# Performance work log

Measured on AMD Instinct MI355X. Metric: run time of the kernel, lower is better.

Reference implementation:

```python
import jax, jax.numpy as jnp
import numpy as np

T, H, I, E, TOPK = 4096, 2048, 4096, 8, 2


def setup_inputs() -> dict:
    key = jax.random.key(0)
    k0, k1, k2, k3, k4, k5 = jax.random.split(key, 6)
    return {
        "hidden_states": jax.random.normal(k0, (T, H), dtype=jnp.float32),
        "expert_affinities": jax.random.uniform(k1, (T, E), dtype=jnp.float32),
        "expert_index": jax.random.randint(k2, (T, TOPK), 0, E),
        "w_gate": jax.random.normal(k3, (E, H, I), dtype=jnp.float32) / np.float32(np.sqrt(H)),
        "w_up": jax.random.normal(k4, (E, H, I), dtype=jnp.float32) / np.float32(np.sqrt(H)),
        "w_down": jax.random.normal(k5, (E, I, H), dtype=jnp.float32) / np.float32(np.sqrt(I)),
    }


def reference(hidden_states, expert_affinities, expert_index, w_gate, w_up, w_down):
    num_experts = w_gate.shape[0]
    # top_k-hot mask (T, E); duplicate expert picks accumulate, matching torch loop
    expert_mask = jnp.sum(jax.nn.one_hot(expert_index, num_experts, dtype=jnp.float32), axis=1)
    # mask affinities to chosen experts, then L1-normalize (F.normalize p=1, eps=1e-12)
    aff = jnp.where(expert_mask == 0, 0.0, expert_affinities)
    aff = aff / jnp.maximum(jnp.sum(jnp.abs(aff), axis=1, keepdims=True), 1e-12)
    # all-experts GLU MLP: every expert processes all tokens
    g = jnp.einsum('th,ehi->eti', hidden_states, w_gate)   # (E, T, I)
    u = jnp.einsum('th,ehi->eti', hidden_states, w_up)     # (E, T, I)
    h = jax.nn.silu(g) * u                                  # (E, T, I)
    out_e = jnp.einsum('eti,eih->eth', h, w_down)           # (E, T, H)
    # affinity-weighted combine across experts
    return jnp.einsum('eth,te->th', out_e, aff)             # (T, H)
```

## Files before the change

kernel.cpp:

```cpp
#include <hip/hip_runtime.h>
#include <hip/hip_bf16.h>


constexpr int kT   = 4096;
constexpr int kH   = 2048;
constexpr int kI   = 4096;
constexpr int kE   = 8;
constexpr int kCap = 4096;
constexpr int kRowsCap = 10240;

typedef __attribute__((ext_vector_type(8))) short bf16x8;
typedef __attribute__((ext_vector_type(4))) float f32x4;

constexpr size_t HSB_OFF  = 0;
constexpr size_t CNT_OFF  = 16777216;
constexpr size_t OFF_OFF  = CNT_OFF + 4096;
constexpr size_t LTOK_OFF = OFF_OFF + 4096;
constexpr size_t LW_OFF   = LTOK_OFF + (size_t)kE * kCap * 4;
constexpr size_t POS_OFF  = LW_OFF + (size_t)kE * kCap * 4;
constexpr size_t WROW_OFF = POS_OFF + (size_t)kT * 2 * 4;
constexpr size_t HBUF_OFF = 17825792;
constexpr size_t RA_OFF   = HBUF_OFF + (size_t)kRowsCap * kI * 2;
constexpr size_t WMAT_B   = (size_t)kE * kH * kI * 2;
constexpr size_t RB_OFF   = RA_OFF + WMAT_B;
constexpr size_t WD_OFF   = RB_OFF + WMAT_B;
constexpr size_t WS_NEED  = WD_OFF + WMAT_B;

__device__ __forceinline__ unsigned short f2bf(float x) {
  unsigned int u = __float_as_uint(x);
  u += 0x7FFFu + ((u >> 16) & 1u);
  return (unsigned short)(u >> 16);
}
__device__ __forceinline__ unsigned pk2(float a, float b) {
  return (unsigned)f2bf(a) | ((unsigned)f2bf(b) << 16);
}
__device__ __forceinline__ float silu_f(float x) { return x / (1.f + __expf(-x)); }

__device__ __forceinline__ void async_copy16(void* lds, const void* g) {
  __builtin_amdgcn_global_load_lds(
      (const __attribute__((address_space(1))) void*)g,
      (__attribute__((address_space(3))) void*)lds, 16, 0, 0);
}

#define MFMA_BF16 __builtin_amdgcn_mfma_f32_16x16x32_bf16

__global__ void cvt_hs_kernel(const float* __restrict__ in, unsigned short* __restrict__ out) {
  size_t i = ((size_t)blockIdx.x * 256 + threadIdx.x) * 8;
  float4 a = *(const float4*)(in + i);
  float4 b = *(const float4*)(in + i + 4);
  uint4 v;
  v.x = pk2(a.x, a.y); v.y = pk2(a.z, a.w);
  v.z = pk2(b.x, b.y); v.w = pk2(b.z, b.w);
  *(uint4*)(out + i) = v;
}

__global__ __launch_bounds__(256)
void tcvt_kernel(const float* __restrict__ src, unsigned short* __restrict__ dst,
                 int K, int N) {
  __shared__ __attribute__((aligned(16))) unsigned short s[64][72];
  const size_t mat = (size_t)K * N;
  const float* S = src + (size_t)blockIdx.z * mat;
  unsigned short* D = dst + (size_t)blockIdx.z * mat;
  const int k0 = blockIdx.y * 64, n0 = blockIdx.x * 64;
  const int t  = threadIdx.x;
  const int n4 = (t & 15) * 4;
  const int k4 = (t >> 4) * 4;
  const float* p0 = S + (size_t)(k0 + k4) * N + n0 + n4;
  float4 r0 = *(const float4*)(p0);
  float4 r1 = *(const float4*)(p0 + N);
  float4 r2 = *(const float4*)(p0 + 2 * (size_t)N);
  float4 r3 = *(const float4*)(p0 + 3 * (size_t)N);
  uint2 v;
  v.x = pk2(r0.x, r1.x); v.y = pk2(r2.x, r3.x); *(uint2*)(&s[n4 + 0][k4]) = v;
  v.x = pk2(r0.y, r1.y); v.y = pk2(r2.y, r3.y); *(uint2*)(&s[n4 + 1][k4]) = v;
  v.x = pk2(r0.z, r1.z); v.y = pk2(r2.z, r3.z); *(uint2*)(&s[n4 + 2][k4]) = v;
  v.x = pk2(r0.w, r1.w); v.y = pk2(r2.w, r3.w); *(uint2*)(&s[n4 + 3][k4]) = v;
  __syncthreads();
  const int nn = t >> 3;
  const int kc = (t & 7) * 8;
#pragma unroll
  for (int i = 0; i < 2; ++i) {
    const int n = nn + i * 32;
    uint4 u = *(const uint4*)(&s[n][kc]);
    *(uint4*)(D + (size_t)(n0 + n) * K + k0 + kc) = u;
  }
}

__global__ void route_kernel(const float* __restrict__ aff, const int* __restrict__ idx,
                             int* counts, int* ltok, float* lw, int* pos) {
  int t = blockIdx.x * 256 + threadIdx.x;
  if (t >= kT) return;
  int e0 = idx[t * 2 + 0];
  int e1 = idx[t * 2 + 1];
  float a0 = aff[t * kE + e0];
  float a1 = aff[t * kE + e1];
  if (e0 == e1) {
    float w = a0 / fmaxf(fabsf(a0), 1e-12f);
    int s = atomicAdd(&counts[e0], 1);
    ltok[e0 * kCap + s] = t;
    lw[e0 * kCap + s]   = w;
    pos[t * 2 + 0] = (e0 << 12) | s;
    pos[t * 2 + 1] = -1;
  } else {
    float d = fmaxf(fabsf(a0) + fabsf(a1), 1e-12f);
    int s0 = atomicAdd(&counts[e0], 1);
    ltok[e0 * kCap + s0] = t;
    lw[e0 * kCap + s0]   = a0 / d;
    int s1 = atomicAdd(&counts[e1], 1);
    ltok[e1 * kCap + s1] = t;
    lw[e1 * kCap + s1]   = a1 / d;
    pos[t * 2 + 0] = (e0 << 12) | s0;
    pos[t * 2 + 1] = (e1 << 12) | s1;
  }
}

__global__ void prefix_kernel(const int* __restrict__ counts, int* offs) {
  if (threadIdx.x == 0 && blockIdx.x == 0) {
    int acc = 0;
    for (int e = 0; e < kE; ++e) { offs[e] = acc; acc += (counts[e] + 255) & ~255; }
  }
}

__global__ void wrow_kernel(const int* __restrict__ counts, const int* __restrict__ offs,
                            const float* __restrict__ lw, float* __restrict__ wrow) {
  int idx = blockIdx.x * 256 + threadIdx.x;
  int e = idx >> 12, s = idx & 4095;
  int cnt = counts[e];
  int al  = (cnt + 255) & ~255;
  if (s < al) wrow[offs[e] + s] = (s < cnt) ? lw[e * kCap + s] : 0.f;
}

__device__ __forceinline__ void wd_path(const float* __restrict__ wd,
                                        unsigned short* __restrict__ wdT,
                                        int xp, int y, int z, int tid, char* ldsraw) {
  const int q  = xp + 64 * y;
  const int kt = q & 63, np = q >> 6;
  const int K = kI, N = kH;
  const float* S = wd + (size_t)z * K * N;
  unsigned short* D = wdT + (size_t)z * K * N;
  const int sub = tid >> 8, t = tid & 255;
  const int k0 = kt * 64, n0 = np * 128 + sub * 64;
  unsigned short (*s)[72] = (unsigned short(*)[72])(ldsraw + sub * 9216);
  const int n4 = (t & 15) * 4;
  const int k4 = (t >> 4) * 4;
  const float* p0 = S + (size_t)(k0 + k4) * N + n0 + n4;
  float4 r0 = *(const float4*)(p0);
  float4 r1 = *(const float4*)(p0 + N);
  float4 r2 = *(const float4*)(p0 + 2 * (size_t)N);
  float4 r3 = *(const float4*)(p0 + 3 * (size_t)N);
  uint2 v;
  v.x = pk2(r0.x, r1.x); v.y = pk2(r2.x, r3.x); *(uint2*)(&s[n4 + 0][k4]) = v;
  v.x = pk2(r0.y, r1.y); v.y = pk2(r2.y, r3.y); *(uint2*)(&s[n4 + 1][k4]) = v;
  v.x = pk2(r0.z, r1.z); v.y = pk2(r2.z, r3.z); *(uint2*)(&s[n4 + 2][k4]) = v;
  v.x = pk2(r0.w, r1.w); v.y = pk2(r2.w, r3.w); *(uint2*)(&s[n4 + 3][k4]) = v;
  __syncthreads();
  const int nn = t >> 3;
  const int kc = (t & 7) * 8;
#pragma unroll
  for (int i = 0; i < 2; ++i) {
    const int n = nn + i * 32;
    uint4 u = *(const uint4*)(&s[n][kc]);
    *(uint4*)(D + (size_t)(n0 + n) * K + k0 + kc) = u;
  }
}

__global__ __launch_bounds__(512, 2)
void gemm_gu_kernel(const unsigned short* __restrict__ hsb,
                    const unsigned short* __restrict__ wgT,
                    const unsigned short* __restrict__ wuT,
                    const int* __restrict__ counts, const int* __restrict__ offs,
                    const int* __restrict__ ltok, const float* __restrict__ wrow,
                    unsigned short* __restrict__ hbuf,
                    const float* __restrict__ wdSrc,
                    unsigned short* __restrict__ wdDst) {
  constexpr int NT = kH / 64;
  __shared__ __attribute__((aligned(16))) unsigned short lds[2 * 32768];

  if (blockIdx.x >= 32) {
    wd_path(wdSrc, wdDst, blockIdx.x - 32, blockIdx.y, blockIdx.z,
            threadIdx.x, (char*)lds);
    return;
  }

  const int e   = blockIdx.z;
  const int cnt = counts[e];
  const int m0  = blockIdx.y * 256;
  if (m0 >= cnt) return;
  const int n0   = blockIdx.x * 128;
  const int tid  = threadIdx.x;
  const int lane = tid & 63;
  const int wv   = tid >> 6;
  const int wm   = wv >> 2;
  const int wn   = wv & 3;
  const int baseRow = offs[e] + m0;

  const int skof = ((tid & 7) ^ ((tid >> 3) & 7)) * 8;
  const int r_   = tid >> 3;
  int s0 = m0 + r_;        s0 = s0 < cnt ? s0 : cnt - 1;
  int s1 = m0 + 64 + r_;   s1 = s1 < cnt ? s1 : cnt - 1;
  int s2 = m0 + 128 + r_;  s2 = s2 < cnt ? s2 : cnt - 1;
  int s3 = m0 + 192 + r_;  s3 = s3 < cnt ? s3 : cnt - 1;
  const unsigned short* aP0 = hsb + (size_t)ltok[e * kCap + s0] * kH + skof;
  const unsigned short* aP1 = hsb + (size_t)ltok[e * kCap + s1] * kH + skof;
  const unsigned short* aP2 = hsb + (size_t)ltok[e * kCap + s2] * kH + skof;
  const unsigned short* aP3 = hsb + (size_t)ltok[e * kCap + s3] * kH + skof;
  const unsigned short* wgP0 = wgT + (size_t)e * kI * kH + (size_t)(n0 + r_) * kH + skof;
  const unsigned short* wgP1 = wgT + (size_t)e * kI * kH + (size_t)(n0 + 64 + r_) * kH + skof;
  const unsigned short* wuP0 = wuT + (size_t)e * kI * kH + (size_t)(n0 + r_) * kH + skof;
  const unsigned short* wuP1 = wuT + (size_t)e * kI * kH + (size_t)(n0 + 64 + r_) * kH + skof;

  char* ldsb = (char*)lds;
  const int stO0 = tid * 16;
  const int stO1 = tid * 16 + 8192;
  const int ar  = lane & 15;
  const int lg  = lane >> 4;
  const int sk0 = ((lg ^ (lane & 7)) << 4);
  const int sk1 = (((4 + lg) ^ (lane & 7)) << 4);

  f32x4 accG[8][2] = {};
  f32x4 accU[8][2] = {};
  bf16x8 a0[4][2], a1[4][2], wgf[2][2], wuf[2][2];

#define STG2(dst, p0, p1, tt) {                                   \
    async_copy16((dst) + stO0, (p0) + (size_t)(tt) * 64);         \
    async_copy16((dst) + stO1, (p1) + (size_t)(tt) * 64); }
#define RD_A(dst, base, mh) _Pragma("unroll")                                  \
  for (int mf = 0; mf < 4; ++mf) {                                             \
    const char* rp_ = (base) + ((mh) * 128 + wm * 64 + mf * 16 + ar) * 128;    \
    dst[mf][0] = *(const bf16x8*)(rp_ + sk0);                                  \
    dst[mf][1] = *(const bf16x8*)(rp_ + sk1); }
#define RD_W(dst, base) _Pragma("unroll")                                      \
  for (int nf = 0; nf < 2; ++nf) {                                             \
    const char* rp_ = (base) + (wn * 32 + nf * 16 + ar) * 128;                 \
    dst[nf][0] = *(const bf16x8*)(rp_ + sk0);                                  \
    dst[nf][1] = *(const bf16x8*)(rp_ + sk1); }
#define MMA16(ACC, W, A, MH)                                                   \
  __builtin_amdgcn_s_setprio(1);                                               \
  _Pragma("unroll") for (int mf = 0; mf < 4; ++mf)                             \
    _Pragma("unroll") for (int nf = 0; nf < 2; ++nf) {                         \
      ACC[(MH)*4+mf][nf] = MFMA_BF16(W[nf][0], A[mf][0], ACC[(MH)*4+mf][nf], 0, 0, 0); \
      ACC[(MH)*4+mf][nf] = MFMA_BF16(W[nf][1], A[mf][1], ACC[(MH)*4+mf][nf], 0, 0, 0); \
    }                                                                          \
  __builtin_amdgcn_s_setprio(0);

#define GU_TILE(t, SA1, SM, VM)                                                \
  {                                                                            \
    char* bc = ldsb + ((t) & 1) * 65536;                                       \
    char* bo = ldsb + (((t) + 1) & 1) * 65536;                                 \
    RD_A(a0, bc, 0); RD_W(wgf, bc + 32768);                                    \
    if (SA1) STG2(bo + 16384, aP2, aP3, (t) + 1);                              \
    __builtin_amdgcn_s_barrier();                                              \
    MMA16(accG, wgf, a0, 0);                                                   \
    __builtin_amdgcn_s_barrier();                                              \
    RD_W(wuf, bc + 49152);                                                     \
    if (SM) STG2(bc, aP0, aP1, (t) + 2);                                       \
    __builtin_amdgcn_s_barrier();                                              \
    MMA16(accU, wuf, a0, 0);                                                   \
    __builtin_amdgcn_s_barrier();                                              \
    RD_A(a1, bc, 1);                                                           \
    if (SM) STG2(bc + 32768, wgP0, wgP1, (t) + 2);                             \
    __builtin_amdgcn_s_barrier();                                              \
    MMA16(accG, wgf, a1, 1);                                                   \
    __builtin_amdgcn_s_barrier();                                              \
    if (SM) STG2(bc + 49152, wuP0, wuP1, (t) + 2);                             \
    __builtin_amdgcn_s_barrier();                                              \
    MMA16(accU, wuf, a1, 1);                                                   \
    if ((VM) >= 0) {                                                           \
      asm volatile("s_waitcnt vmcnt(%0)" :: "i"((VM) < 0 ? 0 : (VM)) : "memory"); \
      __builtin_amdgcn_s_barrier();                                            \
    }                                                                          \
  }

  {
    char* b0 = ldsb;
    char* b1 = ldsb + 65536;
    STG2(b0,         aP0, aP1, 0);
    STG2(b0 + 16384, aP2, aP3, 0);
    STG2(b0 + 32768, wgP0, wgP1, 0);
    STG2(b0 + 49152, wuP0, wuP1, 0);
    STG2(b1,         aP0, aP1, 1);
    STG2(b1 + 32768, wgP0, wgP1, 1);
    STG2(b1 + 49152, wuP0, wuP1, 1);
    asm volatile("s_waitcnt vmcnt(6)" ::: "memory");
    __builtin_amdgcn_s_barrier();
  }

  for (int t = 0; t < NT - 2; ++t) GU_TILE(t, 1, 1, 6);
  GU_TILE(NT - 2, 1, 0, 0);
  GU_TILE(NT - 1, 0, 0, -1);
#undef GU_TILE

  const int lr4 = lg * 4;
#pragma unroll
  for (int mh = 0; mh < 2; ++mh)
#pragma unroll
    for (int mf = 0; mf < 4; ++mf) {
      const int grow = baseRow + mh * 128 + wm * 64 + mf * 16 + ar;
      const float wf = wrow[grow];
#pragma unroll
      for (int nf = 0; nf < 2; ++nf) {
        const int n = n0 + wn * 32 + nf * 16 + lr4;
        f32x4 g = accG[mh * 4 + mf][nf], u = accU[mh * 4 + mf][nf];
        float h0 = silu_f(g[0]) * u[0] * wf;
        float h1 = silu_f(g[1]) * u[1] * wf;
        float h2 = silu_f(g[2]) * u[2] * wf;
        float h3 = silu_f(g[3]) * u[3] * wf;
        uint2 v;
        v.x = pk2(h0, h1);
        v.y = pk2(h2, h3);
        *(uint2*)(hbuf + ((size_t)grow * kI + n)) = v;
      }
    }
#undef STG2
#undef RD_A
#undef RD_W
#undef MMA16
}

__global__ __launch_bounds__(512, 2)
void gemm_dn_kernel(const unsigned short* __restrict__ hbuf,
                    const unsigned short* __restrict__ wdT,
                    const int* __restrict__ counts, const int* __restrict__ offs,
                    float* __restrict__ obuf) {
  constexpr int NT = kI / 64;
  __shared__ __attribute__((aligned(16))) unsigned short lds[2 * 24576];

  const int e   = blockIdx.z;
  const int cnt = counts[e];
  const int m0  = blockIdx.y * 256;
  if (m0 >= cnt) return;
  const int n0   = blockIdx.x * 128;
  const int tid  = threadIdx.x;
  const int lane = tid & 63;
  const int wv   = tid >> 6;
  const int wm   = wv >> 2;
  const int wn   = wv & 3;
  const int baseRow = offs[e] + m0;

  const int skof = ((tid & 7) ^ ((tid >> 3) & 7)) * 8;
  const int r_   = tid >> 3;
  const unsigned short* aP0 = hbuf + (size_t)(baseRow + r_) * kI + skof;
  const unsigned short* aP1 = hbuf + (size_t)(baseRow + 64 + r_) * kI + skof;
  const unsigned short* aP2 = hbuf + (size_t)(baseRow + 128 + r_) * kI + skof;
  const unsigned short* aP3 = hbuf + (size_t)(baseRow + 192 + r_) * kI + skof;
  const unsigned short* wB = wdT + (size_t)e * kH * kI;
  const unsigned short* wP0 = wB + (size_t)(n0 + r_) * kI + skof;
  const unsigned short* wP1 = wB + (size_t)(n0 + 64 + r_) * kI + skof;

  char* ldsb = (char*)lds;
  const int stO0 = tid * 16;
  const int stO1 = tid * 16 + 8192;
  const int ar  = lane & 15;
  const int lg  = lane >> 4;
  const int sk0 = ((lg ^ (lane & 7)) << 4);
  const int sk1 = (((4 + lg) ^ (lane & 7)) << 4);

  f32x4 acc[8][2] = {};
  bf16x8 a0[4][2], a1[4][2], w0[2][2];

#define STG2(dst, p0, p1, tt) {                                   \
    async_copy16((dst) + stO0, (p0) + (size_t)(tt) * 64);         \
    async_copy16((dst) + stO1, (p1) + (size_t)(tt) * 64); }
#define RD_A(dst, base, mh) _Pragma("unroll")                                  \
  for (int mf = 0; mf < 4; ++mf) {                                             \
    const char* rp_ = (base) + ((mh) * 128 + wm * 64 + mf * 16 + ar) * 128;    \
    dst[mf][0] = *(const bf16x8*)(rp_ + sk0);                                  \
    dst[mf][1] = *(const bf16x8*)(rp_ + sk1); }
#define RD_W(dst, base) _Pragma("unroll")                                      \
  for (int nf = 0; nf < 2; ++nf) {                                             \
    const char* rp_ = (base) + 32768 + (wn * 32 + nf * 16 + ar) * 128;         \
    dst[nf][0] = *(const bf16x8*)(rp_ + sk0);                                  \
    dst[nf][1] = *(const bf16x8*)(rp_ + sk1); }
#define MMA16(A, MH)                                                           \
  __builtin_amdgcn_s_setprio(1);                                               \
  _Pragma("unroll") for (int mf = 0; mf < 4; ++mf)                             \
    _Pragma("unroll") for (int nf = 0; nf < 2; ++nf) {                         \
      acc[(MH)*4+mf][nf] = MFMA_BF16(w0[nf][0], A[mf][0], acc[(MH)*4+mf][nf], 0, 0, 0); \
      acc[(MH)*4+mf][nf] = MFMA_BF16(w0[nf][1], A[mf][1], acc[(MH)*4+mf][nf], 0, 0, 0); \
    }                                                                          \
  __builtin_amdgcn_s_setprio(0);

#define DN_TILE(t, SA1, SM, VM)                                                \
  {                                                                            \
    char* bc = ldsb + ((t) & 1) * 49152;                                       \
    char* bo = ldsb + (((t) + 1) & 1) * 49152;                                 \
    RD_A(a0, bc, 0); RD_W(w0, bc);                                             \
    if (SA1) STG2(bo + 16384, aP2, aP3, (t) + 1);                              \
    __builtin_amdgcn_s_barrier();                                              \
    MMA16(a0, 0);                                                              \
    __builtin_amdgcn_s_barrier();                                              \
    RD_A(a1, bc, 1);                                                           \
    if (SM) { STG2(bc, aP0, aP1, (t) + 2);                                     \
              STG2(bc + 32768, wP0, wP1, (t) + 2); }                           \
    __builtin_amdgcn_s_barrier();                                              \
    MMA16(a1, 1);                                                              \
    if ((VM) >= 0) {                                                           \
      asm volatile("s_waitcnt vmcnt(%0)" :: "i"((VM) < 0 ? 0 : (VM)) : "memory"); \
      __builtin_amdgcn_s_barrier();                                            \
    }                                                                          \
  }

  {
    char* b0 = ldsb;
    char* b1 = ldsb + 49152;
    STG2(b0,         aP0, aP1, 0);
    STG2(b0 + 16384, aP2, aP3, 0);
    STG2(b0 + 32768, wP0, wP1, 0);
    STG2(b1,         aP0, aP1, 1);
    STG2(b1 + 32768, wP0, wP1, 1);
    asm volatile("s_waitcnt vmcnt(4)" ::: "memory");
    __builtin_amdgcn_s_barrier();
  }

  for (int t = 0; t < NT - 2; ++t) DN_TILE(t, 1, 1, 4);
  DN_TILE(NT - 2, 1, 0, 0);
  DN_TILE(NT - 1, 0, 0, -1);
#undef DN_TILE

  const int lr4 = lg * 4;
#pragma unroll
  for (int mh = 0; mh < 2; ++mh)
#pragma unroll
    for (int mf = 0; mf < 4; ++mf) {
      const int grow = baseRow + mh * 128 + wm * 64 + mf * 16 + ar;
#pragma unroll
      for (int nf = 0; nf < 2; ++nf) {
        const int n = n0 + wn * 32 + nf * 16 + lr4;
        *(f32x4*)(obuf + (size_t)grow * kH + n) = acc[mh * 4 + mf][nf];
      }
    }
#undef STG2
#undef RD_A
#undef RD_W
#undef MMA16
}

__global__ void combine_kernel(const float* __restrict__ obuf,
                               const int* __restrict__ pos,
                               const int* __restrict__ offs,
                               float* __restrict__ out) {
  const int t   = blockIdx.y;
  const int col = blockIdx.x * 1024 + threadIdx.x * 4;
  const int c0  = pos[t * 2 + 0];
  const int c1  = pos[t * 2 + 1];
  const int row0 = offs[c0 >> 12] + (c0 & 4095);
  float4 v = *(const float4*)(obuf + (size_t)row0 * kH + col);
  if (c1 >= 0) {
    const int row1 = offs[c1 >> 12] + (c1 & 4095);
    float4 w = *(const float4*)(obuf + (size_t)row1 * kH + col);
    v.x += w.x; v.y += w.y; v.z += w.z; v.w += w.w;
  }
  *(float4*)(out + (size_t)t * kH + col) = v;
}

extern "C" void kernel_launch(void* const* d_in, const int* in_sizes, int n_in,
                              void* d_out, int out_size, void* d_ws, size_t ws_size,
                              hipStream_t stream) {
  const float* hs   = (const float*)d_in[0];
  const float* aff  = (const float*)d_in[1];
  const int*   eidx = (const int*)d_in[2];
  const float* wg   = (const float*)d_in[3];
  const float* wu   = (const float*)d_in[4];
  const float* wd   = (const float*)d_in[5];
  float* out = (float*)d_out;

  char* ws = (char*)d_ws;
  unsigned short* hsb  = (unsigned short*)(ws + HSB_OFF);
  unsigned short* hbuf = (unsigned short*)(ws + HBUF_OFF);
  unsigned short* wgT  = (unsigned short*)(ws + RA_OFF);
  unsigned short* wuT  = (unsigned short*)(ws + RB_OFF);
  int*            cnts = (int*)(ws + CNT_OFF);
  int*            offs = (int*)(ws + OFF_OFF);
  int*            ltok = (int*)(ws + LTOK_OFF);
  float*          lwgt = (float*)(ws + LW_OFF);
  int*            pos  = (int*)(ws + POS_OFF);
  float*          wrow = (float*)(ws + WROW_OFF);

  const bool fused = (ws_size >= WS_NEED);
  unsigned short* wdT  = fused ? (unsigned short*)(ws + WD_OFF)
                               : (unsigned short*)(ws + RA_OFF);
  float*          obuf = fused ? (float*)(ws + RA_OFF)
                               : (float*)(ws + RB_OFF);

  hipMemsetAsync(cnts, 0, kE * sizeof(int), stream);

  cvt_hs_kernel<<<(kT * kH) / (256 * 8), 256, 0, stream>>>(hs, hsb);
  route_kernel<<<kT / 256, 256, 0, stream>>>(aff, eidx, cnts, ltok, lwgt, pos);
  prefix_kernel<<<1, 64, 0, stream>>>(cnts, offs);
  wrow_kernel<<<(kE * kCap) / 256, 256, 0, stream>>>(cnts, offs, lwgt, wrow);

  tcvt_kernel<<<dim3(kI / 64, kH / 64, kE), 256, 0, stream>>>(wg, wgT, kH, kI);
  tcvt_kernel<<<dim3(kI / 64, kH / 64, kE), 256, 0, stream>>>(wu, wuT, kH, kI);

  if (fused) {
    gemm_gu_kernel<<<dim3(96, kCap / 256, kE), 512, 0, stream>>>(
        hsb, wgT, wuT, cnts, offs, ltok, wrow, hbuf, wd, wdT);
  } else {
    gemm_gu_kernel<<<dim3(32, kCap / 256, kE), 512, 0, stream>>>(
        hsb, wgT, wuT, cnts, offs, ltok, wrow, hbuf, nullptr, nullptr);
    tcvt_kernel<<<dim3(kH / 64, kI / 64, kE), 256, 0, stream>>>(wd, wdT, kI, kH);
  }

  gemm_dn_kernel<<<dim3(kH / 128, kCap / 256, kE), 512, 0, stream>>>(
      hbuf, wdT, cnts, offs, obuf);

  combine_kernel<<<dim3(kH / 1024, kT), 256, 0, stream>>>(obuf, pos, offs, out);
}
```

Baseline: 718.2 us.

## Shrink down-projection GEMM M-tile to 128 rows for higher occupancy

The down-projection GEMM tile drops from 256x128 to 128x128. LDS use per block falls from 96KB to 64KB, the accumulator register footprint halves, and launch bounds now target 4 blocks per CU. The staging schedule is reworked: the mid-tile A prefetch is dropped, and the next-next tile is now loaded after both MMA halves instead of between them. The aim is better load balance across ragged expert counts and more latency hiding, at the cost of less weight reuse per loaded tile and more global traffic for the weight matrix.

Result: faster. 689.2 us (-4.0%).

```diff
diff --git a/kernel.cpp b/kernel.cpp
--- a/kernel.cpp
+++ b/kernel.cpp
@@ -317,17 +317,17 @@
 #undef MMA16
 }
 
-__global__ __launch_bounds__(512, 2)
+__global__ __launch_bounds__(512, 4)
 void gemm_dn_kernel(const unsigned short* __restrict__ hbuf,
                     const unsigned short* __restrict__ wdT,
                     const int* __restrict__ counts, const int* __restrict__ offs,
                     float* __restrict__ obuf) {
   constexpr int NT = kI / 64;
-  __shared__ __attribute__((aligned(16))) unsigned short lds[2 * 24576];
+  __shared__ __attribute__((aligned(16))) unsigned short lds[2 * 16384];
 
   const int e   = blockIdx.z;
   const int cnt = counts[e];
-  const int m0  = blockIdx.y * 256;
+  const int m0  = blockIdx.y * 128;
   if (m0 >= cnt) return;
   const int n0   = blockIdx.x * 128;
   const int tid  = threadIdx.x;
@@ -341,8 +341,6 @@
   const int r_   = tid >> 3;
   const unsigned short* aP0 = hbuf + (size_t)(baseRow + r_) * kI + skof;
   const unsigned short* aP1 = hbuf + (size_t)(baseRow + 64 + r_) * kI + skof;
-  const unsigned short* aP2 = hbuf + (size_t)(baseRow + 128 + r_) * kI + skof;
-  const unsigned short* aP3 = hbuf + (size_t)(baseRow + 192 + r_) * kI + skof;
   const unsigned short* wB = wdT + (size_t)e * kH * kI;
   const unsigned short* wP0 = wB + (size_t)(n0 + r_) * kI + skof;
   const unsigned short* wP1 = wB + (size_t)(n0 + 64 + r_) * kI + skof;
@@ -355,45 +353,43 @@
   const int sk0 = ((lg ^ (lane & 7)) << 4);
   const int sk1 = (((4 + lg) ^ (lane & 7)) << 4);
 
-  f32x4 acc[8][2] = {};
-  bf16x8 a0[4][2], a1[4][2], w0[2][2];
+  f32x4 acc[4][2] = {};
+  bf16x8 a0[2][2], a1[2][2], w0[2][2];
 
 #define STG2(dst, p0, p1, tt) {                                   \
     async_copy16((dst) + stO0, (p0) + (size_t)(tt) * 64);         \
     async_copy16((dst) + stO1, (p1) + (size_t)(tt) * 64); }
-#define RD_A(dst, base, mh) _Pragma("unroll")                                  \
-  for (int mf = 0; mf < 4; ++mf) {                                             \
-    const char* rp_ = (base) + ((mh) * 128 + wm * 64 + mf * 16 + ar) * 128;    \
+#define RD_A2(dst, base, mp) _Pragma("unroll")                                 \
+  for (int mf = 0; mf < 2; ++mf) {                                             \
+    const char* rp_ = (base) + (wm * 64 + ((mp) * 2 + mf) * 16 + ar) * 128;    \
     dst[mf][0] = *(const bf16x8*)(rp_ + sk0);                                  \
     dst[mf][1] = *(const bf16x8*)(rp_ + sk1); }
 #define RD_W(dst, base) _Pragma("unroll")                                      \
   for (int nf = 0; nf < 2; ++nf) {                                             \
-    const char* rp_ = (base) + 32768 + (wn * 32 + nf * 16 + ar) * 128;         \
+    const char* rp_ = (base) + 16384 + (wn * 32 + nf * 16 + ar) * 128;         \
     dst[nf][0] = *(const bf16x8*)(rp_ + sk0);                                  \
     dst[nf][1] = *(const bf16x8*)(rp_ + sk1); }
-#define MMA16(A, MH)                                                           \
+#define MMA8(A, MP)                                                            \
   __builtin_amdgcn_s_setprio(1);                                               \
-  _Pragma("unroll") for (int mf = 0; mf < 4; ++mf)                             \
+  _Pragma("unroll") for (int mf = 0; mf < 2; ++mf)                             \
     _Pragma("unroll") for (int nf = 0; nf < 2; ++nf) {                         \
-      acc[(MH)*4+mf][nf] = MFMA_BF16(w0[nf][0], A[mf][0], acc[(MH)*4+mf][nf], 0, 0, 0); \
-      acc[(MH)*4+mf][nf] = MFMA_BF16(w0[nf][1], A[mf][1], acc[(MH)*4+mf][nf], 0, 0, 0); \
+      acc[(MP)*2+mf][nf] = MFMA_BF16(w0[nf][0], A[mf][0], acc[(MP)*2+mf][nf], 0, 0, 0); \
+      acc[(MP)*2+mf][nf] = MFMA_BF16(w0[nf][1], A[mf][1], acc[(MP)*2+mf][nf], 0, 0, 0); \
     }                                                                          \
   __builtin_amdgcn_s_setprio(0);
 
-#define DN_TILE(t, SA1, SM, VM)                                                \
+#define DN_TILE(t, SM, VM)                                                     \
   {                                                                            \
-    char* bc = ldsb + ((t) & 1) * 49152;                                       \
-    char* bo = ldsb + (((t) + 1) & 1) * 49152;                                 \
-    RD_A(a0, bc, 0); RD_W(w0, bc);                                             \
-    if (SA1) STG2(bo + 16384, aP2, aP3, (t) + 1);                              \
-    __builtin_amdgcn_s_barrier();                                              \
-    MMA16(a0, 0);                                                              \
-    __builtin_amdgcn_s_barrier();                                              \
-    RD_A(a1, bc, 1);                                                           \
+    char* bc = ldsb + ((t) & 1) * 32768;                                       \
+    RD_A2(a0, bc, 0); RD_W(w0, bc);                                            \
+    __builtin_amdgcn_s_barrier();                                              \
+    MMA8(a0, 0);                                                               \
+    __builtin_amdgcn_s_barrier();                                              \
+    RD_A2(a1, bc, 1);                                                          \
+    __builtin_amdgcn_s_barrier();                                              \
+    MMA8(a1, 1);                                                               \
     if (SM) { STG2(bc, aP0, aP1, (t) + 2);                                     \
-              STG2(bc + 32768, wP0, wP1, (t) + 2); }                           \
-    __builtin_amdgcn_s_barrier();                                              \
-    MMA16(a1, 1);                                                              \
+              STG2(bc + 16384, wP0, wP1, (t) + 2); }                           \
     if ((VM) >= 0) {                                                           \
       asm volatile("s_waitcnt vmcnt(%0)" :: "i"((VM) < 0 ? 0 : (VM)) : "memory"); \
       __builtin_amdgcn_s_barrier();                                            \
@@ -402,37 +398,34 @@
 
   {
     char* b0 = ldsb;
-    char* b1 = ldsb + 49152;
+    char* b1 = ldsb + 32768;
     STG2(b0,         aP0, aP1, 0);
-    STG2(b0 + 16384, aP2, aP3, 0);
-    STG2(b0 + 32768, wP0, wP1, 0);
+    STG2(b0 + 16384, wP0, wP1, 0);
     STG2(b1,         aP0, aP1, 1);
-    STG2(b1 + 32768, wP0, wP1, 1);
+    STG2(b1 + 16384, wP0, wP1, 1);
     asm volatile("s_waitcnt vmcnt(4)" ::: "memory");
     __builtin_amdgcn_s_barrier();
   }
 
-  for (int t = 0; t < NT - 2; ++t) DN_TILE(t, 1, 1, 4);
-  DN_TILE(NT - 2, 1, 0, 0);
-  DN_TILE(NT - 1, 0, 0, -1);
+  for (int t = 0; t < NT - 2; ++t) DN_TILE(t, 1, 4);
+  DN_TILE(NT - 2, 0, 0);
+  DN_TILE(NT - 1, 0, -1);
 #undef DN_TILE
 
   const int lr4 = lg * 4;
 #pragma unroll
-  for (int mh = 0; mh < 2; ++mh)
-#pragma unroll
-    for (int mf = 0; mf < 4; ++mf) {
-      const int grow = baseRow + mh * 128 + wm * 64 + mf * 16 + ar;
-#pragma unroll
-      for (int nf = 0; nf < 2; ++nf) {
-        const int n = n0 + wn * 32 + nf * 16 + lr4;
-        *(f32x4*)(obuf + (size_t)grow * kH + n) = acc[mh * 4 + mf][nf];
-      }
+  for (int mf = 0; mf < 4; ++mf) {
+    const int grow = baseRow + wm * 64 + mf * 16 + ar;
+#pragma unroll
+    for (int nf = 0; nf < 2; ++nf) {
+      const int n = n0 + wn * 32 + nf * 16 + lr4;
+      *(f32x4*)(obuf + (size_t)grow * kH + n) = acc[mf][nf];
     }
+  }
 #undef STG2
-#undef RD_A
+#undef RD_A2
 #undef RD_W
-#undef MMA16
+#undef MMA8
 }
 
 __global__ void combine_kernel(const float* __restrict__ obuf,
@@ -501,7 +494,7 @@
     tcvt_kernel<<<dim3(kH / 64, kI / 64, kE), 256, 0, stream>>>(wd, wdT, kI, kH);
   }
 
-  gemm_dn_kernel<<<dim3(kH / 128, kCap / 256, kE), 512, 0, stream>>>(
+  gemm_dn_kernel<<<dim3(kH / 128, kCap / 128, kE), 512, 0, stream>>>(
       hbuf, wdT, cnts, offs, obuf);
 
   combine_kernel<<<dim3(kH / 1024, kT), 256, 0, stream>>>(obuf, pos, offs, out);
```
